# Kernel tuning notes

Hardware: AMD Instinct MI355X
Metric: run time of the kernel (lower is better)

Reference implementation:

```python
import jax, jax.numpy as jnp
import numpy as np

NA = 100000   # author nodes
NP = 100000   # paper nodes
E = 500000    # edges per relation
H = 128       # hidden size
FA = 256      # author input features
FP = 128      # paper input features
LA = 4        # author labels
LP = 7        # paper labels


def setup_inputs() -> dict:
    key = jax.random.key(0)
    ks = iter(jax.random.split(key, 48))
    def rn(shape, scale=0.05):
        return jax.random.normal(next(ks), shape, jnp.float32) * scale
    inp = {}
    inp['x_author'] = jax.random.normal(next(ks), (NA, FA), jnp.float32)
    inp['x_paper'] = jax.random.normal(next(ks), (NP, FP), jnp.float32)
    inp['edge_index_p2a'] = jax.random.randint(next(ks), (2, E), 0, 100000, jnp.int64)  # row0: paper src, row1: author dst
    inp['edge_index_a2p'] = jax.random.randint(next(ks), (2, E), 0, 100000, jnp.int64)  # row0: author src, row1: paper dst
    # layer 1 convs (per message type): lin_src, lin_dst, lin_update(2H->H)
    inp['w1_p2a_src'] = rn((FP, H)); inp['b1_p2a_src'] = rn((H,))
    inp['w1_p2a_dst'] = rn((FA, H)); inp['b1_p2a_dst'] = rn((H,))
    inp['w1_p2a_upd'] = rn((2 * H, H)); inp['b1_p2a_upd'] = rn((H,))
    inp['w1_a2p_src'] = rn((FA, H)); inp['b1_a2p_src'] = rn((H,))
    inp['w1_a2p_dst'] = rn((FP, H)); inp['b1_a2p_dst'] = rn((H,))
    inp['w1_a2p_upd'] = rn((2 * H, H)); inp['b1_a2p_upd'] = rn((H,))
    # layer 2 convs (all dims = H)
    inp['w2_p2a_src'] = rn((H, H)); inp['b2_p2a_src'] = rn((H,))
    inp['w2_p2a_dst'] = rn((H, H)); inp['b2_p2a_dst'] = rn((H,))
    inp['w2_p2a_upd'] = rn((2 * H, H)); inp['b2_p2a_upd'] = rn((H,))
    inp['w2_a2p_src'] = rn((H, H)); inp['b2_a2p_src'] = rn((H,))
    inp['w2_a2p_dst'] = rn((H, H)); inp['b2_a2p_dst'] = rn((H,))
    inp['w2_a2p_upd'] = rn((2 * H, H)); inp['b2_a2p_upd'] = rn((H,))
    # batchnorm affine params per node type per layer
    inp['g1_a'] = jnp.ones((H,), jnp.float32); inp['be1_a'] = jnp.zeros((H,), jnp.float32)
    inp['g1_p'] = jnp.ones((H,), jnp.float32); inp['be1_p'] = jnp.zeros((H,), jnp.float32)
    inp['g2_a'] = jnp.ones((H,), jnp.float32); inp['be2_a'] = jnp.zeros((H,), jnp.float32)
    inp['g2_p'] = jnp.ones((H,), jnp.float32); inp['be2_p'] = jnp.zeros((H,), jnp.float32)
    # post message-passing heads
    inp['w_post_a'] = rn((H, LA)); inp['b_post_a'] = rn((LA,))
    inp['w_post_p'] = rn((H, LP)); inp['b_post_p'] = rn((LP,))
    return inp


def _mean_agg(x_src, src, dst, n_dst):
    # gather source features along edges, mean-scatter to destination nodes
    msg = x_src[src]                                            # [E, F]
    s = jax.ops.segment_sum(msg, dst, num_segments=n_dst)       # [n_dst, F]
    cnt = jax.ops.segment_sum(jnp.ones((dst.shape[0],), msg.dtype), dst, num_segments=n_dst)
    return s / jnp.maximum(cnt, 1.0)[:, None]


def _conv(x_src, x_dst, src, dst, ws, bs, wd, bd, wu, bu):
    agg = _mean_agg(x_src, src, dst, x_dst.shape[0])
    h = jnp.concatenate([x_dst @ wd + bd, agg @ ws + bs], axis=-1)   # [n_dst, 2H]
    return h @ wu + bu


def _bn_lrelu(x, g, b):
    # BatchNorm1d(eps=1) in training mode (batch stats, biased var) then LeakyReLU(0.01)
    m = x.mean(axis=0)
    v = x.var(axis=0)
    y = g * (x - m) / jnp.sqrt(v + 1.0) + b
    return jnp.where(y >= 0, y, 0.01 * y)


def reference(x_author, x_paper, edge_index_p2a, edge_index_a2p,
              w1_p2a_src, b1_p2a_src, w1_p2a_dst, b1_p2a_dst, w1_p2a_upd, b1_p2a_upd,
              w1_a2p_src, b1_a2p_src, w1_a2p_dst, b1_a2p_dst, w1_a2p_upd, b1_a2p_upd,
              w2_p2a_src, b2_p2a_src, w2_p2a_dst, b2_p2a_dst, w2_p2a_upd, b2_p2a_upd,
              w2_a2p_src, b2_a2p_src, w2_a2p_dst, b2_a2p_dst, w2_a2p_upd, b2_a2p_upd,
              g1_a, be1_a, g1_p, be1_p, g2_a, be2_a, g2_p, be2_p,
              w_post_a, b_post_a, w_post_p, b_post_p):
    src_pa, dst_pa = edge_index_p2a[0], edge_index_p2a[1]
    src_ap, dst_ap = edge_index_a2p[0], edge_index_a2p[1]
    # layer 1: per-message-type conv -> per-node-type BN + LeakyReLU
    h_a = _conv(x_paper, x_author, src_pa, dst_pa, w1_p2a_src, b1_p2a_src, w1_p2a_dst, b1_p2a_dst, w1_p2a_upd, b1_p2a_upd)
    h_p = _conv(x_author, x_paper, src_ap, dst_ap, w1_a2p_src, b1_a2p_src, w1_a2p_dst, b1_a2p_dst, w1_a2p_upd, b1_a2p_upd)
    h_a = _bn_lrelu(h_a, g1_a, be1_a)
    h_p = _bn_lrelu(h_p, g1_p, be1_p)
    # layer 2
    h_a2 = _conv(h_p, h_a, src_pa, dst_pa, w2_p2a_src, b2_p2a_src, w2_p2a_dst, b2_p2a_dst, w2_p2a_upd, b2_p2a_upd)
    h_p2 = _conv(h_a, h_p, src_ap, dst_ap, w2_a2p_src, b2_a2p_src, w2_a2p_dst, b2_a2p_dst, w2_a2p_upd, b2_a2p_upd)
    h_a2 = _bn_lrelu(h_a2, g2_a, be2_a)
    h_p2 = _bn_lrelu(h_p2, g2_p, be2_p)
    # post message-passing heads per node type
    out_a = h_a2 @ w_post_a + b_post_a   # [NA, LA]
    out_p = h_p2 @ w_post_p + b_post_p   # [NP, LP]
    return (out_a, out_p)
```

## Files before the change

### kernel.cpp

```cpp
#include <hip/hip_runtime.h>

#define NN 100000
#define NE 500000
#define HD 128
#define NBLK 391

typedef float f32x4v __attribute__((ext_vector_type(4)));
typedef short s16x8  __attribute__((ext_vector_type(8)));

static __device__ __forceinline__ unsigned f2bf_bits(float f){
  unsigned u = __float_as_uint(f);
  return (u + 0x7FFF + ((u >> 16) & 1)) >> 16;
}
static __device__ __forceinline__ float bfu(unsigned short u){
  return __uint_as_float(((unsigned)u) << 16);
}
static __device__ __forceinline__ float4 recon4(ushort4 h, ushort4 l){
  return make_float4(bfu(h.x)+bfu(l.x), bfu(h.y)+bfu(l.y),
                     bfu(h.z)+bfu(l.z), bfu(h.w)+bfu(l.w));
}
static __device__ __forceinline__ void split4(float4 v, ushort4& h, ushort4& l){
  unsigned hb;
  hb = f2bf_bits(v.x); h.x = (unsigned short)hb; l.x = (unsigned short)f2bf_bits(v.x - __uint_as_float(hb<<16));
  hb = f2bf_bits(v.y); h.y = (unsigned short)hb; l.y = (unsigned short)f2bf_bits(v.y - __uint_as_float(hb<<16));
  hb = f2bf_bits(v.z); h.z = (unsigned short)hb; l.z = (unsigned short)f2bf_bits(v.z - __uint_as_float(hb<<16));
  hb = f2bf_bits(v.w); h.w = (unsigned short)hb; l.w = (unsigned short)f2bf_bits(v.w - __uint_as_float(hb<<16));
}
static __device__ __forceinline__ void split8v(f32x4v v0, f32x4v v1, s16x8& hi, s16x8& lo){
  #pragma unroll
  for (int j = 0; j < 4; ++j){
    float f = v0[j];
    unsigned hb = f2bf_bits(f);
    hi[j] = (short)hb; lo[j] = (short)f2bf_bits(f - __uint_as_float(hb << 16));
  }
  #pragma unroll
  for (int j = 0; j < 4; ++j){
    float f = v1[j];
    unsigned hb = f2bf_bits(f);
    hi[4+j] = (short)hb; lo[4+j] = (short)f2bf_bits(f - __uint_as_float(hb << 16));
  }
}

static __device__ __forceinline__ float4 bn_lrelu4(float4 v, float4 sc, float4 sh){
  v.x = v.x*sc.x + sh.x; v.x = v.x >= 0.f ? v.x : 0.01f*v.x;
  v.y = v.y*sc.y + sh.y; v.y = v.y >= 0.f ? v.y : 0.01f*v.y;
  v.z = v.z*sc.z + sh.z; v.z = v.z >= 0.f ? v.z : 0.01f*v.z;
  v.w = v.w*sc.w + sh.w; v.w = v.w >= 0.f ? v.w : 0.01f*v.w;
  return v;
}

__global__ void k_count(const int* __restrict__ ei_pa, const int* __restrict__ ei_ap,
                        int* __restrict__ deg2){
  int idx = blockIdx.x * 256 + threadIdx.x;
  if (idx < NE)        atomicAdd(&deg2[      ei_pa[NE + idx]], 1);
  else if (idx < 2*NE) atomicAdd(&deg2[NN + ei_ap[NE + (idx - NE)]], 1);
}

__global__ void k_bsum(const int* __restrict__ deg2, int* __restrict__ bsum){
  int rel = blockIdx.x / NBLK, b = blockIdx.x % NBLK;
  int i = b*256 + threadIdx.x;
  int v = (i < NN) ? deg2[rel*NN + i] : 0;
  __shared__ int s[256];
  s[threadIdx.x] = v; __syncthreads();
  for (int o = 128; o > 0; o >>= 1){
    if (threadIdx.x < o) s[threadIdx.x] += s[threadIdx.x + o];
    __syncthreads();
  }
  if (threadIdx.x == 0) bsum[rel*512 + b] = s[0];
}

__global__ void k_bscan(const int* __restrict__ bsum, int* __restrict__ bsoff){
  int rel = blockIdx.x, t = threadIdx.x;
  int v = (t < NBLK) ? bsum[rel*512 + t] : 0;
  __shared__ int s[512];
  s[t] = v; __syncthreads();
  for (int o = 1; o < 512; o <<= 1){
    int x = (t >= o) ? s[t - o] : 0;
    __syncthreads();
    s[t] += x;
    __syncthreads();
  }
  bsoff[rel*512 + t] = s[t] - v;
}

__global__ void k_scanC(const int* __restrict__ deg2, const int* __restrict__ bsoff,
                        int* __restrict__ off2, int* __restrict__ cur2){
  int rel = blockIdx.x / NBLK, b = blockIdx.x % NBLK;
  int i = b*256 + threadIdx.x, t = threadIdx.x;
  int v = (i < NN) ? deg2[rel*NN + i] : 0;
  __shared__ int s[256];
  s[t] = v; __syncthreads();
  for (int o = 1; o < 256; o <<= 1){
    int x = (t >= o) ? s[t - o] : 0;
    __syncthreads();
    s[t] += x;
    __syncthreads();
  }
  if (i < NN){
    int o = bsoff[rel*512 + b] + s[t] - v;
    off2[rel*NN + i] = o;
    cur2[rel*NN + i] = o;
  }
}

__global__ void k_fill(const int* __restrict__ ei_pa, const int* __restrict__ ei_ap,
                       int* __restrict__ cur2,
                       int* __restrict__ col_pa, int* __restrict__ col_ap){
  int idx = blockIdx.x * 256 + threadIdx.x;
  if (idx < NE){
    int s = ei_pa[idx], d = ei_pa[NE + idx];
    int pos = atomicAdd(&cur2[d], 1);
    col_pa[pos] = s;
  } else if (idx < 2*NE){
    int e = idx - NE;
    int s = ei_ap[e], d = ei_ap[NE + e];
    int pos = atomicAdd(&cur2[NN + d], 1);
    col_ap[pos] = s;
  }
}

struct FoldDesc { const float* A; const float* B; short* T; int off; };
struct FoldArgs { FoldDesc d[8]; int rs[9]; };

__global__ void k_fold(FoldArgs fa){
  int row = blockIdx.x;
  int seg = 0;
  #pragma unroll
  for (int s = 0; s < 8; ++s) if (row >= fa.rs[s+1]) seg = s + 1;
  int m = row - fa.rs[seg];
  const float* A = fa.d[seg].A + (size_t)m * 128;
  const float* B = fa.d[seg].B;
  int n = threadIdx.x;
  float acc = 0.f;
  for (int k = 0; k < 128; ++k) acc += A[k] * B[k*128 + n];
  unsigned hb = f2bf_bits(acc);
  float hf = __uint_as_float(hb << 16);
  unsigned lb = f2bf_bits(acc - hf);
  int gkc = fa.d[seg].off + (m >> 5), quad = (m >> 3) & 3, j = m & 7;
  int lane = quad*16 + (n & 15), nt = n >> 4;
  size_t fb = (size_t)((gkc*8 + nt)*2)*512 + lane*8 + j;
  fa.d[seg].T[fb]       = (short)hb;
  fa.d[seg].T[fb + 512] = (short)lb;
}

struct BiasArgs { const float* bd[4]; const float* bs[4]; const float* wu[4];
                  const float* bu[4]; float* outb[4]; };
__global__ void k_biasfold(BiasArgs ba){
  int s = blockIdx.x, j = threadIdx.x;
  const float* wu = ba.wu[s];
  float acc = ba.bu[s][j];
  for (int k = 0; k < 128; ++k)
    acc += ba.bd[s][k] * wu[k*128 + j] + ba.bs[s][k] * wu[(128 + k)*128 + j];
  ba.outb[s][j] = acc;
}

template<int SPLITA1>
__global__ __launch_bounds__(256)
void k_gemm2(const void* __restrict__ A1v, int K1, int KC1,
             const ushort* __restrict__ A2, int K2, int KC2,
             const short* __restrict__ Bf,
             const float* __restrict__ bias, const ushort* __restrict__ extra,
             ushort* __restrict__ C, float* __restrict__ stats, int M)
{
  __shared__ __align__(16) char smem[32768];
  short* Bs = (short*)smem;

  const int tid  = threadIdx.x;
  const int wave = tid >> 6, lane = tid & 63;
  const int li   = lane & 15, quad = lane >> 4;
  const int rowT = blockIdx.x * 128 + wave * 32;
  const int KCtot = KC1 + KC2;

  f32x4v acc[2][8];
  #pragma unroll
  for (int mt = 0; mt < 2; ++mt)
    #pragma unroll
    for (int nt = 0; nt < 8; ++nt)
      acc[mt][nt] = (f32x4v){0.f, 0.f, 0.f, 0.f};

  const char*   b1[2];
  const ushort* b2[2];
  #pragma unroll
  for (int mt = 0; mt < 2; ++mt){
    int row = rowT + mt*16 + li;
    int r = (row < M) ? row : 0;
    if (SPLITA1) b1[mt] = (const char*)((const ushort*)A1v + (size_t)r*(2*K1) + quad*8);
    else         b1[mt] = (const char*)((const float*) A1v + (size_t)r*K1     + quad*8);
    b2[mt] = A2 ? (A2 + (size_t)r*(2*K2) + quad*8) : (const ushort*)nullptr;
  }

  f32x4v aA[2][2][2], aB[2][2][2];

  auto loadA = [&](int g, f32x4v (&dst)[2][2][2]){
    #pragma unroll
    for (int kc = 0; kc < 2; ++kc){
      int gkc = g + kc;
      #pragma unroll
      for (int mt = 0; mt < 2; ++mt){
        if (gkc < KC1){
          if (SPLITA1){
            const ushort* p = (const ushort*)b1[mt] + gkc*32;
            dst[kc][mt][0] = *(const f32x4v*)p;
            dst[kc][mt][1] = *(const f32x4v*)(p + K1);
          } else {
            const float* p = (const float*)b1[mt] + gkc*32;
            dst[kc][mt][0] = *(const f32x4v*)p;
            dst[kc][mt][1] = *(const f32x4v*)(p + 4);
          }
        } else {
          const ushort* p = b2[mt] + (gkc - KC1)*32;
          dst[kc][mt][0] = *(const f32x4v*)p;
          dst[kc][mt][1] = *(const f32x4v*)(p + K2);
        }
      }
    }
  };

  auto stageB = [&](int g){
    const char* s = (const char*)Bf + (size_t)g * 16384;
    #pragma unroll
    for (int c = 0; c < 8; ++c){
      int blk = wave*8 + c;
      __builtin_amdgcn_global_load_lds(
          (const __attribute__((address_space(1))) unsigned int*)(s + blk*1024 + lane*16),
          (__attribute__((address_space(3))) unsigned int*)(smem + blk*1024),
          16, 0, 0);
    }
  };

  auto computeG = [&](int g, f32x4v (&a)[2][2][2]){
    bool f32g = (!SPLITA1) && (g < KC1);
    #pragma unroll
    for (int kc = 0; kc < 2; ++kc){
      s16x8 ah[2], al[2];
      if (f32g){
        #pragma unroll
        for (int mt = 0; mt < 2; ++mt)
          split8v(a[kc][mt][0], a[kc][mt][1], ah[mt], al[mt]);
      } else {
        #pragma unroll
        for (int mt = 0; mt < 2; ++mt){
          ah[mt] = __builtin_bit_cast(s16x8, a[kc][mt][0]);
          al[mt] = __builtin_bit_cast(s16x8, a[kc][mt][1]);
        }
      }
      #pragma unroll
      for (int nt = 0; nt < 8; ++nt){
        const short* bp = Bs + ((kc*8 + nt) << 10) + lane*8;
        s16x8 bh = *(const s16x8*)bp;
        s16x8 bl = *(const s16x8*)(bp + 512);
        #pragma unroll
        for (int mt = 0; mt < 2; ++mt){
          acc[mt][nt] = __builtin_amdgcn_mfma_f32_16x16x32_bf16(ah[mt], bh, acc[mt][nt], 0, 0, 0);
          acc[mt][nt] = __builtin_amdgcn_mfma_f32_16x16x32_bf16(al[mt], bh, acc[mt][nt], 0, 0, 0);
          acc[mt][nt] = __builtin_amdgcn_mfma_f32_16x16x32_bf16(ah[mt], bl, acc[mt][nt], 0, 0, 0);
        }
      }
    }
  };

  auto phase = [&](int G, f32x4v (&cur)[2][2][2], f32x4v (&nxt)[2][2][2]){
    if (G) __syncthreads();
    stageB(G);
    __syncthreads();
    if (G + 2 < KCtot) loadA(G + 2, nxt);
    computeG(G, cur);
  };

  loadA(0, aA);
  for (int g = 0; g < KCtot; g += 4){
    phase(g,     aA, aB);
    phase(g + 2, aB, aA);
  }

  __syncthreads();
  float* Cw = (float*)smem + wave*2048;
  int col4 = lane & 31;
  float4 bias4 = make_float4(0.f,0.f,0.f,0.f);
  if (bias) bias4 = ((const float4*)bias)[col4];
  float4 s1 = make_float4(0.f,0.f,0.f,0.f), s2 = s1;
  #pragma unroll
  for (int mt = 0; mt < 2; ++mt){
    #pragma unroll
    for (int r = 0; r < 4; ++r){
      int lr = quad*4 + r;
      #pragma unroll
      for (int nt = 0; nt < 8; ++nt){
        int c = nt*16 + li;
        int chunk = ((c >> 2) + 2*quad) & 31;
        Cw[lr*128 + chunk*4 + (c & 3)] = acc[mt][nt][r];
      }
    }
    #pragma unroll
    for (int i = 0; i < 8; ++i){
      int lr = i*2 + (lane >> 5);
      int grow = rowT + mt*16 + lr;
      if (grow >= M) continue;
      int chunk = (col4 + 2*(lr >> 2)) & 31;
      float4 v = *(const float4*)(Cw + lr*128 + chunk*4);
      v.x += bias4.x; v.y += bias4.y; v.z += bias4.z; v.w += bias4.w;
      if (extra){
        const ushort* er = extra + ((size_t)grow << 8) + col4*4;
        ushort4 eh = *(const ushort4*)er;
        ushort4 el = *(const ushort4*)(er + 128);
        float4 e = recon4(eh, el);
        v.x += e.x; v.y += e.y; v.z += e.z; v.w += e.w;
      }
      ushort4 h4, l4; split4(v, h4, l4);
      ushort* cr = C + ((size_t)grow << 8) + col4*4;
      *(ushort4*)cr = h4;
      *(ushort4*)(cr + 128) = l4;
      s1.x += v.x; s1.y += v.y; s1.z += v.z; s1.w += v.w;
      s2.x += v.x*v.x; s2.y += v.y*v.y; s2.z += v.z*v.z; s2.w += v.w*v.w;
    }
  }
  if (stats){
    __syncthreads();
    float* Ss = (float*)smem;
    ((float4*)Ss)[tid*2]     = s1;
    ((float4*)Ss)[tid*2 + 1] = s2;
    __syncthreads();
    int c = tid & 127, kind = tid >> 7;
    int cc4 = c >> 2, comp = c & 3;
    float s = 0.f;
    #pragma unroll
    for (int wv = 0; wv < 4; ++wv)
      #pragma unroll
      for (int hf = 0; hf < 2; ++hf)
        s += Ss[(wv*64 + hf*32 + cc4)*8 + kind*4 + comp];
    atomicAdd(&stats[kind*128 + c], s);
  }
}

template<int IS>
__global__ __launch_bounds__(256)
void k_agg(const void* __restrict__ tv, const int* __restrict__ off,
           const int* __restrict__ deg, const int* __restrict__ col,
           ushort* __restrict__ o){
  const float*  tf = (const float*)tv;
  const ushort* ts = (const ushort*)tv;
  int slot = threadIdx.x >> 5, col4 = threadIdx.x & 31;
  int d = blockIdx.x*8 + slot;
  if (d >= NN) return;
  auto loadrow = [&](int row) -> float4 {
    if (IS){
      const ushort* p = ts + ((size_t)row << 8) + col4*4;
      ushort4 h = *(const ushort4*)p;
      ushort4 l = *(const ushort4*)(p + 128);
      return recon4(h, l);
    } else {
      return ((const float4*)(tf + ((size_t)row << 7)))[col4];
    }
  };
  int s0 = off[d], cnt = deg[d];
  float4 a0 = make_float4(0.f,0.f,0.f,0.f), a1 = a0;
  int i = 0;
  for (; i + 4 <= cnt; i += 4){
    int sa = col[s0+i], sb = col[s0+i+1], sct = col[s0+i+2], sd = col[s0+i+3];
    float4 v0 = loadrow(sa);
    float4 v1 = loadrow(sb);
    float4 v2 = loadrow(sct);
    float4 v3 = loadrow(sd);
    a0.x += v0.x + v2.x; a0.y += v0.y + v2.y; a0.z += v0.z + v2.z; a0.w += v0.w + v2.w;
    a1.x += v1.x + v3.x; a1.y += v1.y + v3.y; a1.z += v1.z + v3.z; a1.w += v1.w + v3.w;
  }
  for (; i < cnt; ++i){
    float4 v0 = loadrow(col[s0+i]);
    a0.x += v0.x; a0.y += v0.y; a0.z += v0.z; a0.w += v0.w;
  }
  float inv = 1.0f / (float)(cnt > 0 ? cnt : 1);
  float4 r;
  r.x = (a0.x + a1.x)*inv; r.y = (a0.y + a1.y)*inv;
  r.z = (a0.z + a1.z)*inv; r.w = (a0.w + a1.w)*inv;
  ushort4 h4, l4; split4(r, h4, l4);
  ushort* po = o + ((size_t)d << 8) + col4*4;
  *(ushort4*)po = h4;
  *(ushort4*)(po + 128) = l4;
}

__global__ void k_bnprep(const float* __restrict__ stats, const float* __restrict__ g,
                         const float* __restrict__ b, float* __restrict__ sc, int M){
  int c = threadIdx.x;
  float invN = 1.0f / (float)M;
  float m  = stats[c] * invN;
  float var = stats[128 + c] * invN - m*m;
  float scale = g[c] / sqrtf(var + 1.0f);
  sc[c] = scale;
  sc[128 + c] = b[c] - m*scale;
}

__global__ __launch_bounds__(256)
void k_bnapply(ushort* __restrict__ t, const float* __restrict__ bn){
  int i = blockIdx.x*256 + threadIdx.x;
  int row = i >> 5, c4 = i & 31;
  float4 sc = ((const float4*)bn)[c4];
  float4 sh = ((const float4*)(bn + 128))[c4];
  ushort* p = t + ((size_t)row << 8) + c4*4;
  ushort4 h = *(const ushort4*)p;
  ushort4 l = *(const ushort4*)(p + 128);
  float4 v = recon4(h, l);
  v = bn_lrelu4(v, sc, sh);
  split4(v, h, l);
  *(ushort4*)p = h;
  *(ushort4*)(p + 128) = l;
}

template<int LC>
__global__ void k_head(const ushort* __restrict__ h, const float* __restrict__ bn,
                       const float* __restrict__ w, const float* __restrict__ b,
                       float* __restrict__ o, int M){
  __shared__ float ws[128*LC];
  __shared__ float bs[LC];
  __shared__ float bsc[256];
  for (int i = threadIdx.x; i < 128*LC; i += 256) ws[i] = w[i];
  if (threadIdx.x < LC) bs[threadIdx.x] = b[threadIdx.x];
  if (threadIdx.x < 256) bsc[threadIdx.x] = bn[threadIdx.x];
  __syncthreads();
  int r = blockIdx.x*256 + threadIdx.x;
  if (r >= M) return;
  float acc[LC];
  #pragma unroll
  for (int c = 0; c < LC; ++c) acc[c] = bs[c];
  const ushort* hr = h + ((size_t)r << 8);
  for (int k4 = 0; k4 < 32; ++k4){
    ushort4 uh = ((const ushort4*)hr)[k4];
    ushort4 ul = ((const ushort4*)(hr + 128))[k4];
    float4 v = recon4(uh, ul);
    float4 sc = ((const float4*)bsc)[k4];
    float4 sh = ((const float4*)bsc)[32 + k4];
    v = bn_lrelu4(v, sc, sh);
    int k = k4*4;
    #pragma unroll
    for (int c = 0; c < LC; ++c)
      acc[c] += v.x*ws[k*LC+c] + v.y*ws[(k+1)*LC+c] + v.z*ws[(k+2)*LC+c] + v.w*ws[(k+3)*LC+c];
  }
  #pragma unroll
  for (int c = 0; c < LC; ++c) o[(size_t)r*LC + c] = acc[c];
}

extern "C" void kernel_launch(void* const* d_in, const int* in_sizes, int n_in,
                              void* d_out, int out_size, void* d_ws, size_t ws_size,
                              hipStream_t stream) {
  const float* x_author = (const float*)d_in[0];
  const float* x_paper  = (const float*)d_in[1];
  const int*   ei_pa    = (const int*)d_in[2];
  const int*   ei_ap    = (const int*)d_in[3];

  char* p = (char*)d_ws;
  auto alloc = [&](size_t bytes) -> void* {
    void* r = (void*)p; p += (bytes + 255) & ~(size_t)255; return r;
  };
  short* T_l1a  = (short*)alloc(12u*16384);
  short* T_l1ps = (short*)alloc( 8u*16384);
  short* T_l1pd = (short*)alloc( 4u*16384);
  short* T_l2a  = (short*)alloc( 8u*16384);
  short* T_l2p  = (short*)alloc( 8u*16384);
  float* w1a_b = (float*)alloc(128*4);      float* w1p_b = (float*)alloc(128*4);
  float* w2a_b = (float*)alloc(128*4);      float* w2p_b = (float*)alloc(128*4);
  float* stats4 = (float*)alloc(4*256*4);
  float* bnsc4  = (float*)alloc(4*256*4);
  int* deg2  = (int*)alloc(2*NN*4);
  int* off2  = (int*)alloc(2*NN*4);
  int* cur2  = (int*)alloc(2*NN*4);
  int* col_pa = (int*)alloc(NE*4);
  int* col_ap = (int*)alloc(NE*4);
  int* bsum  = (int*)alloc(1024*4);
  int* bsoff = (int*)alloc(1024*4);
  const size_t NB = (size_t)NN * 128;
  ushort* B1 = (ushort*)alloc(NB*4);
  ushort* B2 = (ushort*)alloc(NB*4);
  ushort* B3 = (ushort*)alloc(NB*4);
  ushort* B4 = (ushort*)alloc(NB*4);

  hipMemsetAsync(deg2, 0, 2*NN*4, stream);
  hipMemsetAsync(stats4, 0, 4*256*4, stream);
  k_count<<<(2*NE + 255)/256, 256, 0, stream>>>(ei_pa, ei_ap, deg2);
  k_bsum <<<2*NBLK, 256, 0, stream>>>(deg2, bsum);
  k_bscan<<<2, 512, 0, stream>>>(bsum, bsoff);
  k_scanC<<<2*NBLK, 256, 0, stream>>>(deg2, bsoff, off2, cur2);
  k_fill <<<(2*NE + 255)/256, 256, 0, stream>>>(ei_pa, ei_ap, cur2, col_pa, col_ap);

  FoldArgs fa;
  const float* wu1a = (const float*)d_in[8];
  const float* wu1p = (const float*)d_in[14];
  const float* wu2a = (const float*)d_in[20];
  const float* wu2p = (const float*)d_in[26];
  fa.d[0] = { (const float*)d_in[6],  wu1a,           T_l1a,  0 };
  fa.d[1] = { (const float*)d_in[4],  wu1a + 128*128, T_l1a,  8 };
  fa.d[2] = { (const float*)d_in[10], wu1p + 128*128, T_l1ps, 0 };
  fa.d[3] = { (const float*)d_in[12], wu1p,           T_l1pd, 0 };
  fa.d[4] = { (const float*)d_in[18], wu2a,           T_l2a,  0 };
  fa.d[5] = { (const float*)d_in[16], wu2a + 128*128, T_l2a,  4 };
  fa.d[6] = { (const float*)d_in[24], wu2p,           T_l2p,  0 };
  fa.d[7] = { (const float*)d_in[22], wu2p + 128*128, T_l2p,  4 };
  int rows[8] = {256,128,256,128,128,128,128,128};
  fa.rs[0] = 0;
  for (int i = 0; i < 8; ++i) fa.rs[i+1] = fa.rs[i] + rows[i];
  k_fold<<<fa.rs[8], 128, 0, stream>>>(fa);

  BiasArgs ba;
  ba.bd[0]=(const float*)d_in[7];  ba.bs[0]=(const float*)d_in[5];  ba.wu[0]=wu1a; ba.bu[0]=(const float*)d_in[9];  ba.outb[0]=w1a_b;
  ba.bd[1]=(const float*)d_in[13]; ba.bs[1]=(const float*)d_in[11]; ba.wu[1]=wu1p; ba.bu[1]=(const float*)d_in[15]; ba.outb[1]=w1p_b;
  ba.bd[2]=(const float*)d_in[19]; ba.bs[2]=(const float*)d_in[17]; ba.wu[2]=wu2a; ba.bu[2]=(const float*)d_in[21]; ba.outb[2]=w2a_b;
  ba.bd[3]=(const float*)d_in[25]; ba.bs[3]=(const float*)d_in[23]; ba.wu[3]=wu2p; ba.bu[3]=(const float*)d_in[27]; ba.outb[3]=w2p_b;
  k_biasfold<<<4, 128, 0, stream>>>(ba);

  const int GG = (NN + 127)/128;
  const int AGG_GRID = (NN + 7)/8;
  const int BN_GRID  = (NN*32)/256;
  const int* off_pa = off2;        const int* deg_pa = deg2;
  const int* off_ap = off2 + NN;   const int* deg_ap = deg2 + NN;
  float* st_a1 = stats4;       float* st_p1 = stats4 + 256;
  float* st_a2 = stats4 + 512; float* st_p2 = stats4 + 768;
  float* sc_a1 = bnsc4;        float* sc_p1 = bnsc4 + 256;
  float* sc_a2 = bnsc4 + 512;  float* sc_p2 = bnsc4 + 768;

  k_agg<0><<<AGG_GRID, 256, 0, stream>>>(x_paper, off_pa, deg_pa, col_pa, B4);
  k_gemm2<0><<<GG, 256, 0, stream>>>(x_author, 256, 8, B4, 128, 4, T_l1a,
                                     w1a_b, nullptr, B1, st_a1, NN);
  k_bnprep<<<1, 128, 0, stream>>>(st_a1, (const float*)d_in[28], (const float*)d_in[29], sc_a1, NN);

  k_gemm2<0><<<GG, 256, 0, stream>>>(x_author, 256, 8, nullptr, 0, 0, T_l1ps,
                                     nullptr, nullptr, B3, nullptr, NN);
  k_agg<1><<<AGG_GRID, 256, 0, stream>>>(B3, off_ap, deg_ap, col_ap, B4);
  k_gemm2<0><<<GG, 256, 0, stream>>>(x_paper, 128, 4, nullptr, 0, 0, T_l1pd,
                                     w1p_b, B4, B2, st_p1, NN);
  k_bnprep<<<1, 128, 0, stream>>>(st_p1, (const float*)d_in[30], (const float*)d_in[31], sc_p1, NN);

  k_bnapply<<<BN_GRID, 256, 0, stream>>>(B1, sc_a1);
  k_bnapply<<<BN_GRID, 256, 0, stream>>>(B2, sc_p1);

  k_agg<1><<<AGG_GRID, 256, 0, stream>>>(B2, off_pa, deg_pa, col_pa, B4);
  k_gemm2<1><<<GG, 256, 0, stream>>>(B1, 128, 4, B4, 128, 4, T_l2a,
                                     w2a_b, nullptr, B3, st_a2, NN);
  k_bnprep<<<1, 128, 0, stream>>>(st_a2, (const float*)d_in[32], (const float*)d_in[33], sc_a2, NN);
  k_head<4><<<(NN + 255)/256, 256, 0, stream>>>(B3, sc_a2, (const float*)d_in[36],
                                                (const float*)d_in[37], (float*)d_out, NN);

  k_agg<1><<<AGG_GRID, 256, 0, stream>>>(B1, off_ap, deg_ap, col_ap, B4);
  k_gemm2<1><<<GG, 256, 0, stream>>>(B2, 128, 4, B4, 128, 4, T_l2p,
                                     w2p_b, nullptr, B3, st_p2, NN);
  k_bnprep<<<1, 128, 0, stream>>>(st_p2, (const float*)d_in[34], (const float*)d_in[35], sc_p2, NN);
  k_head<7><<<(NN + 255)/256, 256, 0, stream>>>(B3, sc_p2, (const float*)d_in[38],
                                                (const float*)d_in[39], (float*)d_out + (size_t)NN*4, NN);
}
```

Before: 922.6 us.

## Restructure GEMM to 8 waves with triple-buffered B staging and single-barrier pipeline

The GEMM kernel moves from 4 waves each owning 32 rows to 8 waves each owning 16 rows. The B-weight staging changes from a single LDS buffer loaded in two k-chunks per phase to a 3-deep ring buffer fed one k-chunk ahead, waited on with explicit vmcnt and a single barrier per step. The aim is more latency hiding and fewer barriers per step. The cost is more LDS per block, the epilogue running in two wave-group passes with extra syncs, and halved per-wave B reuse.

```diff
diff --git a/kernel.cpp b/kernel.cpp
--- a/kernel.cpp
+++ b/kernel.cpp
@@ -155,180 +155,163 @@
 }
 
 template<int SPLITA1>
-__global__ __launch_bounds__(256)
+__global__ __launch_bounds__(512)
 void k_gemm2(const void* __restrict__ A1v, int K1, int KC1,
              const ushort* __restrict__ A2, int K2, int KC2,
              const short* __restrict__ Bf,
              const float* __restrict__ bias, const ushort* __restrict__ extra,
              ushort* __restrict__ C, float* __restrict__ stats, int M)
 {
-  __shared__ __align__(16) char smem[32768];
-  short* Bs = (short*)smem;
+  __shared__ __align__(16) char smem[49152];
 
   const int tid  = threadIdx.x;
   const int wave = tid >> 6, lane = tid & 63;
   const int li   = lane & 15, quad = lane >> 4;
-  const int rowT = blockIdx.x * 128 + wave * 32;
+  const int rowT = blockIdx.x * 128 + wave * 16;
   const int KCtot = KC1 + KC2;
 
-  f32x4v acc[2][8];
-  #pragma unroll
-  for (int mt = 0; mt < 2; ++mt)
+  f32x4v acc[8];
+  #pragma unroll
+  for (int nt = 0; nt < 8; ++nt) acc[nt] = (f32x4v){0.f, 0.f, 0.f, 0.f};
+
+  const char*   b1;
+  const ushort* b2;
+  {
+    int row = rowT + li;
+    int r = (row < M) ? row : 0;
+    if (SPLITA1) b1 = (const char*)((const ushort*)A1v + (size_t)r*(2*K1) + quad*8);
+    else         b1 = (const char*)((const float*) A1v + (size_t)r*K1     + quad*8);
+    b2 = A2 ? (A2 + (size_t)r*(2*K2) + quad*8) : (const ushort*)nullptr;
+  }
+
+  auto loadA = [&](int gkc, f32x4v* dst){
+    if (gkc < KC1){
+      if (SPLITA1){
+        const ushort* p = (const ushort*)b1 + gkc*32;
+        dst[0] = *(const f32x4v*)p;
+        dst[1] = *(const f32x4v*)(p + K1);
+      } else {
+        const float* p = (const float*)b1 + gkc*32;
+        dst[0] = *(const f32x4v*)p;
+        dst[1] = *(const f32x4v*)(p + 4);
+      }
+    } else {
+      const ushort* p = b2 + (gkc - KC1)*32;
+      dst[0] = *(const f32x4v*)p;
+      dst[1] = *(const f32x4v*)(p + K2);
+    }
+  };
+
+  auto stageB = [&](int kc, int bufIdx){
+    const char* s = (const char*)Bf + (size_t)kc * 16384;
+    char* d = smem + bufIdx * 16384;
     #pragma unroll
-    for (int nt = 0; nt < 8; ++nt)
-      acc[mt][nt] = (f32x4v){0.f, 0.f, 0.f, 0.f};
-
-  const char*   b1[2];
-  const ushort* b2[2];
-  #pragma unroll
-  for (int mt = 0; mt < 2; ++mt){
-    int row = rowT + mt*16 + li;
-    int r = (row < M) ? row : 0;
-    if (SPLITA1) b1[mt] = (const char*)((const ushort*)A1v + (size_t)r*(2*K1) + quad*8);
-    else         b1[mt] = (const char*)((const float*) A1v + (size_t)r*K1     + quad*8);
-    b2[mt] = A2 ? (A2 + (size_t)r*(2*K2) + quad*8) : (const ushort*)nullptr;
-  }
-
-  f32x4v aA[2][2][2], aB[2][2][2];
-
-  auto loadA = [&](int g, f32x4v (&dst)[2][2][2]){
+    for (int c = 0; c < 2; ++c){
+      int off = c*8192 + wave*1024;
+      __builtin_amdgcn_global_load_lds(
+          (const __attribute__((address_space(1))) unsigned int*)(s + off + lane*16),
+          (__attribute__((address_space(3))) unsigned int*)(d + off),
+          16, 0, 0);
+    }
+  };
+
+  auto computeK = [&](int j, int bufIdx, f32x4v* a){
+    s16x8 ah, al;
+    if ((!SPLITA1) && (j < KC1)) split8v(a[0], a[1], ah, al);
+    else { ah = __builtin_bit_cast(s16x8, a[0]); al = __builtin_bit_cast(s16x8, a[1]); }
+    const short* base = (const short*)(smem + bufIdx*16384) + lane*8;
     #pragma unroll
-    for (int kc = 0; kc < 2; ++kc){
-      int gkc = g + kc;
-      #pragma unroll
-      for (int mt = 0; mt < 2; ++mt){
-        if (gkc < KC1){
-          if (SPLITA1){
-            const ushort* p = (const ushort*)b1[mt] + gkc*32;
-            dst[kc][mt][0] = *(const f32x4v*)p;
-            dst[kc][mt][1] = *(const f32x4v*)(p + K1);
-          } else {
-            const float* p = (const float*)b1[mt] + gkc*32;
-            dst[kc][mt][0] = *(const f32x4v*)p;
-            dst[kc][mt][1] = *(const f32x4v*)(p + 4);
-          }
-        } else {
-          const ushort* p = b2[mt] + (gkc - KC1)*32;
-          dst[kc][mt][0] = *(const f32x4v*)p;
-          dst[kc][mt][1] = *(const f32x4v*)(p + K2);
-        }
-      }
+    for (int nt = 0; nt < 8; ++nt){
+      const short* bp = base + (nt << 10);
+      s16x8 bh = *(const s16x8*)bp;
+      s16x8 bl = *(const s16x8*)(bp + 512);
+      acc[nt] = __builtin_amdgcn_mfma_f32_16x16x32_bf16(ah, bh, acc[nt], 0, 0, 0);
+      acc[nt] = __builtin_amdgcn_mfma_f32_16x16x32_bf16(al, bh, acc[nt], 0, 0, 0);
+      acc[nt] = __builtin_amdgcn_mfma_f32_16x16x32_bf16(ah, bl, acc[nt], 0, 0, 0);
     }
   };
 
-  auto stageB = [&](int g){
-    const char* s = (const char*)Bf + (size_t)g * 16384;
-    #pragma unroll
-    for (int c = 0; c < 8; ++c){
-      int blk = wave*8 + c;
-      __builtin_amdgcn_global_load_lds(
-          (const __attribute__((address_space(1))) unsigned int*)(s + blk*1024 + lane*16),
-          (__attribute__((address_space(3))) unsigned int*)(smem + blk*1024),
-          16, 0, 0);
-    }
-  };
-
-  auto computeG = [&](int g, f32x4v (&a)[2][2][2]){
-    bool f32g = (!SPLITA1) && (g < KC1);
-    #pragma unroll
-    for (int kc = 0; kc < 2; ++kc){
-      s16x8 ah[2], al[2];
-      if (f32g){
-        #pragma unroll
-        for (int mt = 0; mt < 2; ++mt)
-          split8v(a[kc][mt][0], a[kc][mt][1], ah[mt], al[mt]);
-      } else {
-        #pragma unroll
-        for (int mt = 0; mt < 2; ++mt){
-          ah[mt] = __builtin_bit_cast(s16x8, a[kc][mt][0]);
-          al[mt] = __builtin_bit_cast(s16x8, a[kc][mt][1]);
-        }
-      }
-      #pragma unroll
-      for (int nt = 0; nt < 8; ++nt){
-        const short* bp = Bs + ((kc*8 + nt) << 10) + lane*8;
-        s16x8 bh = *(const s16x8*)bp;
-        s16x8 bl = *(const s16x8*)(bp + 512);
-        #pragma unroll
-        for (int mt = 0; mt < 2; ++mt){
-          acc[mt][nt] = __builtin_amdgcn_mfma_f32_16x16x32_bf16(ah[mt], bh, acc[mt][nt], 0, 0, 0);
-          acc[mt][nt] = __builtin_amdgcn_mfma_f32_16x16x32_bf16(al[mt], bh, acc[mt][nt], 0, 0, 0);
-          acc[mt][nt] = __builtin_amdgcn_mfma_f32_16x16x32_bf16(ah[mt], bl, acc[mt][nt], 0, 0, 0);
-        }
-      }
-    }
-  };
-
-  auto phase = [&](int G, f32x4v (&cur)[2][2][2], f32x4v (&nxt)[2][2][2]){
-    if (G) __syncthreads();
-    stageB(G);
-    __syncthreads();
-    if (G + 2 < KCtot) loadA(G + 2, nxt);
-    computeG(G, cur);
-  };
-
-  loadA(0, aA);
-  for (int g = 0; g < KCtot; g += 4){
-    phase(g,     aA, aB);
-    phase(g + 2, aB, aA);
+  f32x4v aC[2], aN1[2], aN2[2];
+  stageB(0, 0); loadA(0, aC);
+  stageB(1, 1); loadA(1, aN1);
+  int bi = 0;
+  for (int j = 0; j < KCtot; ++j){
+    if (j + 1 < KCtot) asm volatile("s_waitcnt vmcnt(4)" ::: "memory");
+    else               asm volatile("s_waitcnt vmcnt(0)" ::: "memory");
+    __builtin_amdgcn_s_barrier();
+    __builtin_amdgcn_sched_barrier(0);
+    if (j + 2 < KCtot){
+      int b2i = bi + 2; if (b2i >= 3) b2i -= 3;
+      stageB(j + 2, b2i);
+      loadA(j + 2, aN2);
+    }
+    computeK(j, bi, aC);
+    aC[0] = aN1[0]; aC[1] = aN1[1];
+    aN1[0] = aN2[0]; aN1[1] = aN2[1];
+    bi = (bi + 1 == 3) ? 0 : bi + 1;
   }
 
   __syncthreads();
-  float* Cw = (float*)smem + wave*2048;
+  float* Cw = (float*)smem + (wave & 3) * 2048;
+  const int grp = wave >> 2;
   int col4 = lane & 31;
   float4 bias4 = make_float4(0.f,0.f,0.f,0.f);
   if (bias) bias4 = ((const float4*)bias)[col4];
   float4 s1 = make_float4(0.f,0.f,0.f,0.f), s2 = s1;
   #pragma unroll
-  for (int mt = 0; mt < 2; ++mt){
-    #pragma unroll
-    for (int r = 0; r < 4; ++r){
-      int lr = quad*4 + r;
+  for (int g2 = 0; g2 < 2; ++g2){
+    if (grp == g2){
       #pragma unroll
-      for (int nt = 0; nt < 8; ++nt){
-        int c = nt*16 + li;
-        int chunk = ((c >> 2) + 2*quad) & 31;
-        Cw[lr*128 + chunk*4 + (c & 3)] = acc[mt][nt][r];
+      for (int r = 0; r < 4; ++r){
+        int lr = quad*4 + r;
+        #pragma unroll
+        for (int nt = 0; nt < 8; ++nt){
+          int c = nt*16 + li;
+          int chunk = ((c >> 2) + 2*quad) & 31;
+          Cw[lr*128 + chunk*4 + (c & 3)] = acc[nt][r];
+        }
       }
-    }
-    #pragma unroll
-    for (int i = 0; i < 8; ++i){
-      int lr = i*2 + (lane >> 5);
-      int grow = rowT + mt*16 + lr;
-      if (grow >= M) continue;
-      int chunk = (col4 + 2*(lr >> 2)) & 31;
-      float4 v = *(const float4*)(Cw + lr*128 + chunk*4);
-      v.x += bias4.x; v.y += bias4.y; v.z += bias4.z; v.w += bias4.w;
-      if (extra){
-        const ushort* er = extra + ((size_t)grow << 8) + col4*4;
-        ushort4 eh = *(const ushort4*)er;
-        ushort4 el = *(const ushort4*)(er + 128);
-        float4 e = recon4(eh, el);
-        v.x += e.x; v.y += e.y; v.z += e.z; v.w += e.w;
+      #pragma unroll
+      for (int i = 0; i < 8; ++i){
+        int lr = i*2 + (lane >> 5);
+        int grow = rowT + lr;
+        if (grow >= M) continue;
+        int chunk = (col4 + 2*(lr >> 2)) & 31;
+        float4 v = *(const float4*)(Cw + lr*128 + chunk*4);
+        v.x += bias4.x; v.y += bias4.y; v.z += bias4.z; v.w += bias4.w;
+        if (extra){
+          const ushort* er = extra + ((size_t)grow << 8) + col4*4;
+          ushort4 eh = *(const ushort4*)er;
+          ushort4 el = *(const ushort4*)(er + 128);
+          float4 e = recon4(eh, el);
+          v.x += e.x; v.y += e.y; v.z += e.z; v.w += e.w;
+        }
+        ushort4 h4, l4; split4(v, h4, l4);
+        ushort* cr = C + ((size_t)grow << 8) + col4*4;
+        *(ushort4*)cr = h4;
+        *(ushort4*)(cr + 128) = l4;
+        s1.x += v.x; s1.y += v.y; s1.z += v.z; s1.w += v.w;
+        s2.x += v.x*v.x; s2.y += v.y*v.y; s2.z += v.z*v.z; s2.w += v.w*v.w;
       }
-      ushort4 h4, l4; split4(v, h4, l4);
-      ushort* cr = C + ((size_t)grow << 8) + col4*4;
-      *(ushort4*)cr = h4;
-      *(ushort4*)(cr + 128) = l4;
-      s1.x += v.x; s1.y += v.y; s1.z += v.z; s1.w += v.w;
-      s2.x += v.x*v.x; s2.y += v.y*v.y; s2.z += v.z*v.z; s2.w += v.w*v.w;
-    }
+    }
+    __syncthreads();
   }
   if (stats){
-    __syncthreads();
     float* Ss = (float*)smem;
     ((float4*)Ss)[tid*2]     = s1;
     ((float4*)Ss)[tid*2 + 1] = s2;
     __syncthreads();
-    int c = tid & 127, kind = tid >> 7;
-    int cc4 = c >> 2, comp = c & 3;
-    float s = 0.f;
-    #pragma unroll
-    for (int wv = 0; wv < 4; ++wv)
+    if (tid < 256){
+      int c = tid & 127, kind = tid >> 7;
+      int cc4 = c >> 2, comp = c & 3;
+      float s = 0.f;
       #pragma unroll
-      for (int hf = 0; hf < 2; ++hf)
-        s += Ss[(wv*64 + hf*32 + cc4)*8 + kind*4 + comp];
-    atomicAdd(&stats[kind*128 + c], s);
+      for (int wv = 0; wv < 8; ++wv)
+        #pragma unroll
+        for (int hf = 0; hf < 2; ++hf)
+          s += Ss[(wv*64 + hf*32 + cc4)*8 + kind*4 + comp];
+      atomicAdd(&stats[kind*128 + c], s);
+    }
   }
 }
 
@@ -516,14 +499,14 @@
   float* sc_a2 = bnsc4 + 512;  float* sc_p2 = bnsc4 + 768;
 
   k_agg<0><<<AGG_GRID, 256, 0, stream>>>(x_paper, off_pa, deg_pa, col_pa, B4);
-  k_gemm2<0><<<GG, 256, 0, stream>>>(x_author, 256, 8, B4, 128, 4, T_l1a,
+  k_gemm2<0><<<GG, 512, 0, stream>>>(x_author, 256, 8, B4, 128, 4, T_l1a,
                                      w1a_b, nullptr, B1, st_a1, NN);
   k_bnprep<<<1, 128, 0, stream>>>(st_a1, (const float*)d_in[28], (const float*)d_in[29], sc_a1, NN);
 
-  k_gemm2<0><<<GG, 256, 0, stream>>>(x_author, 256, 8, nullptr, 0, 0, T_l1ps,
+  k_gemm2<0><<<GG, 512, 0, stream>>>(x_author, 256, 8, nullptr, 0, 0, T_l1ps,
                                      nullptr, nullptr, B3, nullptr, NN);
   k_agg<1><<<AGG_GRID, 256, 0, stream>>>(B3, off_ap, deg_ap, col_ap, B4);
-  k_gemm2<0><<<GG, 256, 0, stream>>>(x_paper, 128, 4, nullptr, 0, 0, T_l1pd,
+  k_gemm2<0><<<GG, 512, 0, stream>>>(x_paper, 128, 4, nullptr, 0, 0, T_l1pd,
                                      w1p_b, B4, B2, st_p1, NN);
   k_bnprep<<<1, 128, 0, stream>>>(st_p1, (const float*)d_in[30], (const float*)d_in[31], sc_p1, NN);
 
@@ -531,14 +514,14 @@
   k_bnapply<<<BN_GRID, 256, 0, stream>>>(B2, sc_p1);
 
   k_agg<1><<<AGG_GRID, 256, 0, stream>>>(B2, off_pa, deg_pa, col_pa, B4);
-  k_gemm2<1><<<GG, 256, 0, stream>>>(B1, 128, 4, B4, 128, 4, T_l2a,
+  k_gemm2<1><<<GG, 512, 0, stream>>>(B1, 128, 4, B4, 128, 4, T_l2a,
                                      w2a_b, nullptr, B3, st_a2, NN);
   k_bnprep<<<1, 128, 0, stream>>>(st_a2, (const float*)d_in[32], (const float*)d_in[33], sc_a2, NN);
   k_head<4><<<(NN + 255)/256, 256, 0, stream>>>(B3, sc_a2, (const float*)d_in[36],
                                                 (const float*)d_in[37], (float*)d_out, NN);
 
   k_agg<1><<<AGG_GRID, 256, 0, stream>>>(B1, off_ap, deg_ap, col_ap, B4);
-  k_gemm2<1><<<GG, 256, 0, stream>>>(B2, 128, 4, B4, 128, 4, T_l2p,
+  k_gemm2<1><<<GG, 512, 0, stream>>>(B2, 128, 4, B4, 128, 4, T_l2p,
                                      w2p_b, nullptr, B3, st_p2, NN);
   k_bnprep<<<1, 128, 0, stream>>>(st_p2, (const float*)d_in[34], (const float*)d_in[35], sc_p2, NN);
   k_head<7><<<(NN + 255)/256, 256, 0, stream>>>(B3, sc_p2, (const float*)d_in[38],
```

New measurement: 901.0 us. -2.3%, faster.

## Triple-buffer B tiles in LDS with per-K-chunk pipeline and vmcnt waits

Applied to the files above, without the earlier changes.

Restructures the GEMM main loop from two-chunk phases with a single LDS buffer and two __syncthreads per phase into a three-slot LDS ring. B staging and A register prefetch run two K-chunks ahead, and a single barrier per chunk follows a partial vmcnt wait. MFMA sections are raised in priority with s_setprio. The aim is to overlap global-to-LDS loads with compute and remove barrier stalls, at the cost of 48KB LDS per block, which may lower occupancy. It also relies on the hand-coded vmcnt count matching the number of outstanding loads.

```diff
diff --git a/kernel.cpp b/kernel.cpp
--- a/kernel.cpp
+++ b/kernel.cpp
@@ -162,8 +162,7 @@
              const float* __restrict__ bias, const ushort* __restrict__ extra,
              ushort* __restrict__ C, float* __restrict__ stats, int M)
 {
-  __shared__ __align__(16) char smem[32768];
-  short* Bs = (short*)smem;
+  __shared__ __align__(16) char smem[49152];
 
   const int tid  = threadIdx.x;
   const int wave = tid >> 6, lane = tid & 63;
@@ -189,88 +188,90 @@
     b2[mt] = A2 ? (A2 + (size_t)r*(2*K2) + quad*8) : (const ushort*)nullptr;
   }
 
-  f32x4v aA[2][2][2], aB[2][2][2];
-
-  auto loadA = [&](int g, f32x4v (&dst)[2][2][2]){
-    #pragma unroll
-    for (int kc = 0; kc < 2; ++kc){
-      int gkc = g + kc;
+  auto loadA = [&](int gkc, f32x4v (&dst)[2][2]){
+    #pragma unroll
+    for (int mt = 0; mt < 2; ++mt){
+      if (gkc < KC1){
+        if (SPLITA1){
+          const ushort* p = (const ushort*)b1[mt] + gkc*32;
+          dst[mt][0] = *(const f32x4v*)p;
+          dst[mt][1] = *(const f32x4v*)(p + K1);
+        } else {
+          const float* p = (const float*)b1[mt] + gkc*32;
+          dst[mt][0] = *(const f32x4v*)p;
+          dst[mt][1] = *(const f32x4v*)(p + 4);
+        }
+      } else {
+        const ushort* p = b2[mt] + (gkc - KC1)*32;
+        dst[mt][0] = *(const f32x4v*)p;
+        dst[mt][1] = *(const f32x4v*)(p + K2);
+      }
+    }
+  };
+
+  auto stageB = [&](int kc, int bufIdx){
+    const char* s = (const char*)Bf + (size_t)kc * 16384;
+    char* d = smem + bufIdx * 16384;
+    #pragma unroll
+    for (int c = 0; c < 4; ++c){
+      int off = c*4096 + wave*1024;
+      __builtin_amdgcn_global_load_lds(
+          (const __attribute__((address_space(1))) unsigned int*)(s + off + lane*16),
+          (__attribute__((address_space(3))) unsigned int*)(d + off),
+          16, 0, 0);
+    }
+  };
+
+  auto computeK = [&](int j, int bufIdx, f32x4v (&a)[2][2]){
+    s16x8 ah[2], al[2];
+    if ((!SPLITA1) && (j < KC1)){
+      #pragma unroll
+      for (int mt = 0; mt < 2; ++mt) split8v(a[mt][0], a[mt][1], ah[mt], al[mt]);
+    } else {
       #pragma unroll
       for (int mt = 0; mt < 2; ++mt){
-        if (gkc < KC1){
-          if (SPLITA1){
-            const ushort* p = (const ushort*)b1[mt] + gkc*32;
-            dst[kc][mt][0] = *(const f32x4v*)p;
-            dst[kc][mt][1] = *(const f32x4v*)(p + K1);
-          } else {
-            const float* p = (const float*)b1[mt] + gkc*32;
-            dst[kc][mt][0] = *(const f32x4v*)p;
-            dst[kc][mt][1] = *(const f32x4v*)(p + 4);
-          }
-        } else {
-          const ushort* p = b2[mt] + (gkc - KC1)*32;
-          dst[kc][mt][0] = *(const f32x4v*)p;
-          dst[kc][mt][1] = *(const f32x4v*)(p + K2);
-        }
+        ah[mt] = __builtin_bit_cast(s16x8, a[mt][0]);
+        al[mt] = __builtin_bit_cast(s16x8, a[mt][1]);
       }
     }
+    const short* base = (const short*)(smem + bufIdx*16384) + lane*8;
+    __builtin_amdgcn_s_setprio(1);
+    #pragma unroll
+    for (int nt = 0; nt < 8; ++nt){
+      const short* bp = base + (nt << 10);
+      s16x8 bh = *(const s16x8*)bp;
+      s16x8 bl = *(const s16x8*)(bp + 512);
+      #pragma unroll
+      for (int mt = 0; mt < 2; ++mt){
+        acc[mt][nt] = __builtin_amdgcn_mfma_f32_16x16x32_bf16(ah[mt], bh, acc[mt][nt], 0, 0, 0);
+        acc[mt][nt] = __builtin_amdgcn_mfma_f32_16x16x32_bf16(al[mt], bh, acc[mt][nt], 0, 0, 0);
+        acc[mt][nt] = __builtin_amdgcn_mfma_f32_16x16x32_bf16(ah[mt], bl, acc[mt][nt], 0, 0, 0);
+      }
+    }
+    __builtin_amdgcn_s_setprio(0);
   };
 
-  auto stageB = [&](int g){
-    const char* s = (const char*)Bf + (size_t)g * 16384;
-    #pragma unroll
-    for (int c = 0; c < 8; ++c){
-      int blk = wave*8 + c;
-      __builtin_amdgcn_global_load_lds(
-          (const __attribute__((address_space(1))) unsigned int*)(s + blk*1024 + lane*16),
-          (__attribute__((address_space(3))) unsigned int*)(smem + blk*1024),
-          16, 0, 0);
-    }
-  };
-
-  auto computeG = [&](int g, f32x4v (&a)[2][2][2]){
-    bool f32g = (!SPLITA1) && (g < KC1);
-    #pragma unroll
-    for (int kc = 0; kc < 2; ++kc){
-      s16x8 ah[2], al[2];
-      if (f32g){
-        #pragma unroll
-        for (int mt = 0; mt < 2; ++mt)
-          split8v(a[kc][mt][0], a[kc][mt][1], ah[mt], al[mt]);
-      } else {
-        #pragma unroll
-        for (int mt = 0; mt < 2; ++mt){
-          ah[mt] = __builtin_bit_cast(s16x8, a[kc][mt][0]);
-          al[mt] = __builtin_bit_cast(s16x8, a[kc][mt][1]);
-        }
-      }
-      #pragma unroll
-      for (int nt = 0; nt < 8; ++nt){
-        const short* bp = Bs + ((kc*8 + nt) << 10) + lane*8;
-        s16x8 bh = *(const s16x8*)bp;
-        s16x8 bl = *(const s16x8*)(bp + 512);
-        #pragma unroll
-        for (int mt = 0; mt < 2; ++mt){
-          acc[mt][nt] = __builtin_amdgcn_mfma_f32_16x16x32_bf16(ah[mt], bh, acc[mt][nt], 0, 0, 0);
-          acc[mt][nt] = __builtin_amdgcn_mfma_f32_16x16x32_bf16(al[mt], bh, acc[mt][nt], 0, 0, 0);
-          acc[mt][nt] = __builtin_amdgcn_mfma_f32_16x16x32_bf16(ah[mt], bl, acc[mt][nt], 0, 0, 0);
-        }
-      }
-    }
-  };
-
-  auto phase = [&](int G, f32x4v (&cur)[2][2][2], f32x4v (&nxt)[2][2][2]){
-    if (G) __syncthreads();
-    stageB(G);
-    __syncthreads();
-    if (G + 2 < KCtot) loadA(G + 2, nxt);
-    computeG(G, cur);
-  };
-
-  loadA(0, aA);
-  for (int g = 0; g < KCtot; g += 4){
-    phase(g,     aA, aB);
-    phase(g + 2, aB, aA);
+  f32x4v aC[2][2], aN1[2][2], aN2[2][2];
+  stageB(0, 0); loadA(0, aC);
+  stageB(1, 1); loadA(1, aN1);
+  int bi = 0;
+  for (int j = 0; j < KCtot; ++j){
+    if (j + 1 < KCtot) asm volatile("s_waitcnt vmcnt(8)" ::: "memory");
+    else               asm volatile("s_waitcnt vmcnt(0)" ::: "memory");
+    __builtin_amdgcn_s_barrier();
+    __builtin_amdgcn_sched_barrier(0);
+    if (j + 2 < KCtot){
+      int b2i = bi + 2; if (b2i >= 3) b2i -= 3;
+      stageB(j + 2, b2i);
+      loadA(j + 2, aN2);
+    }
+    computeK(j, bi, aC);
+    #pragma unroll
+    for (int mt = 0; mt < 2; ++mt){
+      aC[mt][0] = aN1[mt][0]; aC[mt][1] = aN1[mt][1];
+      aN1[mt][0] = aN2[mt][0]; aN1[mt][1] = aN2[mt][1];
+    }
+    bi = (bi + 1 == 3) ? 0 : bi + 1;
   }
 
   __syncthreads();
```

Measured after the change: 901.9 us. 2.2% less time.
